# Optimization experiments

Measured on AMD Instinct MI355X. Metric: run time of the kernel, lower is better.

Reference implementation:

```python
import jax, jax.numpy as jnp
import numpy as np

B, T, C, H = 8, 2048, 768, 12
D = C // H

def setup_inputs() -> dict:
    key = jax.random.key(0)
    ks = jax.random.split(key, 5)
    s = 0.02
    return {
        "x": jax.random.normal(ks[0], (B, T, C), dtype=jnp.float32),
        "w_attn": jax.random.normal(ks[1], (C, 3 * C), dtype=jnp.float32) * s,
        "b_attn": jnp.zeros((3 * C,), dtype=jnp.float32),
        "w_proj": jax.random.normal(ks[2], (C, C), dtype=jnp.float32) * s,
        "b_proj": jnp.zeros((C,), dtype=jnp.float32),
    }

def reference(x, w_attn, b_attn, w_proj, b_proj):
    Bx, Tx, Cx = x.shape
    qkv = x @ w_attn + b_attn                       # [B,T,3C]
    q, k, v = jnp.split(qkv, 3, axis=-1)
    # [B,H,T,D]
    q = q.reshape(Bx, Tx, H, D).transpose(0, 2, 1, 3)
    k = k.reshape(Bx, Tx, H, D).transpose(0, 2, 1, 3)
    v = v.reshape(Bx, Tx, H, D).transpose(0, 2, 1, 3)
    scale = 1.0 / jnp.sqrt(jnp.float32(D))
    att = jnp.einsum('bhqd,bhkd->bhqk', q, k) * scale
    causal = jnp.tril(jnp.ones((Tx, Tx), dtype=bool))
    att = jnp.where(causal[None, None], att, -jnp.inf)
    att = jax.nn.softmax(att, axis=-1)
    y = jnp.einsum('bhqk,bhkd->bhqd', att, v)
    y = y.transpose(0, 2, 1, 3).reshape(Bx, Tx, Cx)
    y = y @ w_proj + b_proj
    return y, k, v
```

## Files before the change

### kernel.cpp

```cpp
#include <hip/hip_runtime.h>
#include <hip/hip_bf16.h>
#include <stdint.h>

#define Bz 8
#define Tz 2048
#define Cz 768
#define Hz 12
#define Dz 64
#define Mz (Bz*Tz)
#define N3 (3*Cz)
#define YSZ ((size_t)Mz*Cz)

#define SCL 0.18033688011112042f
#define KVB 64
#define QBLK 128

typedef __bf16 bf16;
typedef __attribute__((ext_vector_type(8))) bf16 bf16x8;
typedef __attribute__((ext_vector_type(4))) bf16 bf16x4;
typedef __attribute__((ext_vector_type(4))) float f32x4;

#define MFMA(A_,B_,C_) __builtin_amdgcn_mfma_f32_16x16x32_bf16(A_,B_,C_,0,0,0)

__device__ __forceinline__ void gll16(const void* g, void* l) {
  __builtin_amdgcn_global_load_lds(
      (const __attribute__((address_space(1))) void*)g,
      (__attribute__((address_space(3))) void*)l, 16, 0, 0);
}

__global__ __launch_bounds__(256) void prep_x(const float* __restrict__ x,
                                              bf16* __restrict__ xb) {
  int i = blockIdx.x*blockDim.x + threadIdx.x;
  int stride = gridDim.x*blockDim.x;
  const float4* x4 = (const float4*)x;
  int n4 = (int)(YSZ/4);
  for (int j = i; j < n4; j += stride) {
    float4 f = x4[j];
    bf16x4 o = { (bf16)f.x, (bf16)f.y, (bf16)f.z, (bf16)f.w };
    *(bf16x4*)(xb + 4*(size_t)j) = o;
  }
}

__global__ __launch_bounds__(256) void transpose_conv(const float* __restrict__ src,
                                                      bf16* __restrict__ dst,
                                                      int R, int Ncol) {
  __shared__ float tile[32][33];
  int bx = blockIdx.x, by = blockIdx.y;
  int tx = threadIdx.x & 31, ty = threadIdx.x >> 5;
  #pragma unroll
  for (int i = 0; i < 4; ++i)
    tile[ty + 8*i][tx] = src[(size_t)(by*32 + ty + 8*i)*Ncol + bx*32 + tx];
  __syncthreads();
  #pragma unroll
  for (int i = 0; i < 4; ++i)
    dst[(size_t)(bx*32 + ty + 8*i)*R + by*32 + tx] = (bf16)tile[tx][ty + 8*i];
}

template<int EPI>
__global__ __launch_bounds__(256) void gemm128(
    const bf16* __restrict__ A, const bf16* __restrict__ Bt,
    int Kdim, int Mtiles, int Ntiles,
    const float* __restrict__ bias,
    bf16* __restrict__ qws, bf16* __restrict__ kws, bf16* __restrict__ vtb,
    float* __restrict__ kout, float* __restrict__ vout,
    float* __restrict__ yout)
{
  __shared__ alignas(16) bf16 sA[2][128*64];
  __shared__ alignas(16) bf16 sB[2][128*64];
  int nwg = Mtiles*Ntiles;
  int bid = blockIdx.x;
  int cpx = nwg >> 3;
  int swz = (bid & 7)*cpx + (bid >> 3);
  int ntile = swz % Ntiles, mtile = swz / Ntiles;
  int tid = threadIdx.x, w = tid >> 6, l = tid & 63;
  int wr = w >> 1, wc = w & 1;
  const int rowBase = mtile*128, colBase = ntile*128;

  f32x4 acc[4][4] = {};

  int rbase = tid >> 3;
  int ch    = tid & 7;
  int swk   = (ch ^ (rbase & 7)) << 3;
  const bf16* gA = A + (size_t)(rowBase + rbase)*Kdim + swk;
  const bf16* gB = Bt + (size_t)(colBase + rbase)*Kdim + swk;

  int lr = l & 15, lg = l >> 4;
  int nK = Kdim >> 6;

  {
    char* lA = (char*)sA[0] + w*1024;
    char* lB = (char*)sB[0] + w*1024;
    #pragma unroll
    for (int p = 0; p < 4; ++p) {
      gll16(gA + (size_t)(p*32)*Kdim, lA + p*4096);
      gll16(gB + (size_t)(p*32)*Kdim, lB + p*4096);
    }
    gA += 64; gB += 64;
  }
  int buf = 0;
  for (int t = 0; t < nK; ++t) {
    if (t + 1 < nK) {
      char* lA = (char*)sA[buf ^ 1] + w*1024;
      char* lB = (char*)sB[buf ^ 1] + w*1024;
      #pragma unroll
      for (int p = 0; p < 4; ++p) {
        gll16(gA + (size_t)(p*32)*Kdim, lA + p*4096);
        gll16(gB + (size_t)(p*32)*Kdim, lB + p*4096);
      }
      gA += 64; gB += 64;
      asm volatile("s_waitcnt vmcnt(8)" ::: "memory");
    } else {
      asm volatile("s_waitcnt vmcnt(0)" ::: "memory");
    }
    __builtin_amdgcn_s_barrier();
    __builtin_amdgcn_sched_barrier(0);
    const char* cA = (const char*)sA[buf];
    const char* cB = (const char*)sB[buf];
    __builtin_amdgcn_s_setprio(1);
    #pragma unroll
    for (int kk = 0; kk < 2; ++kk) {
      bf16x8 af[4], bfr[4];
      int cc = ((kk*4 + lg) ^ (lr & 7)) << 4;
      #pragma unroll
      for (int m = 0; m < 4; ++m)
        af[m] = *(const bf16x8*)(cA + (wr*64 + m*16 + lr)*128 + cc);
      #pragma unroll
      for (int n = 0; n < 4; ++n)
        bfr[n] = *(const bf16x8*)(cB + (wc*64 + n*16 + lr)*128 + cc);
      #pragma unroll
      for (int m = 0; m < 4; ++m)
        #pragma unroll
        for (int n = 0; n < 4; ++n)
          acc[m][n] = MFMA(af[m], bfr[n], acc[m][n]);
    }
    __builtin_amdgcn_s_setprio(0);
    asm volatile("s_waitcnt lgkmcnt(0)" ::: "memory");
    __builtin_amdgcn_s_barrier();
    __builtin_amdgcn_sched_barrier(0);
    buf ^= 1;
  }

  #pragma unroll
  for (int m = 0; m < 4; ++m) {
    #pragma unroll
    for (int n = 0; n < 4; ++n) {
      int gcol = colBase + wc*64 + n*16 + lr;
      float bv = bias[gcol];
      int grow0 = rowBase + wr*64 + m*16 + lg*4;
      if (EPI == 1) {
        #pragma unroll
        for (int r = 0; r < 4; ++r)
          yout[(size_t)(grow0 + r)*Cz + gcol] = acc[m][n][r] + bv;
      } else {
        int which = gcol / Cz;
        int within = gcol - which*Cz;
        int h = within >> 6, d = within & 63;
        int bidx = grow0 >> 11;
        int t0 = grow0 & 2047;
        size_t bhTD = ((size_t)bidx*Hz + h);
        if (which == 0) {
          bf16* qp = qws + (bhTD*Tz + t0)*Dz + d;
          #pragma unroll
          for (int r = 0; r < 4; ++r)
            qp[(size_t)r*Dz] = (bf16)((acc[m][n][r] + bv) * SCL);
        } else if (which == 1) {
          float* kp = kout + (bhTD*Tz + t0)*Dz + d;
          bf16*  kp2 = kws + (bhTD*Tz + t0)*Dz + d;
          #pragma unroll
          for (int r = 0; r < 4; ++r) {
            float v = acc[m][n][r] + bv;
            kp[(size_t)r*Dz] = v;
            kp2[(size_t)r*Dz] = (bf16)v;
          }
        } else {
          float* vp = vout + (bhTD*Tz + t0)*Dz + d;
          bf16x4 pk;
          #pragma unroll
          for (int r = 0; r < 4; ++r) {
            float v = acc[m][n][r] + bv;
            vp[(size_t)r*Dz] = v;
            pk[r] = (bf16)v;
          }
          int ts = (t0 & ~31) | (((t0 >> 2) & 3) << 3) | (((t0 >> 4) & 1) << 2) | (t0 & 3);
          *(bf16x4*)(vtb + (bhTD*Dz + d)*Tz + ts) = pk;
        }
      }
    }
  }
}

__device__ __forceinline__ void stageKV(const bf16* kgb, const bf16* vgb, int kv0,
                                        char* cK, char* cV, int tid, int w) {
  int off = tid*16;
  int row = off >> 7, ch = (off >> 4) & 7;
  int sw = ((ch ^ (row & 7)) << 3);
  gll16(kgb + (size_t)(kv0 + row)*Dz + sw, cK + w*1024);
  gll16(vgb + (size_t)row*Tz + kv0 + sw,   cV + w*1024);
}

__device__ __forceinline__ void attn_tile(
    int kv0, int qminw, int qmaxw, int q_l, int lr, int lg,
    const char* cK, const char* cV,
    const bf16x8& qf0, const bf16x8& qf1,
    f32x4 (&o)[4], float& mrun, float& lrun)
{
  const f32x4 zf = {0.f, 0.f, 0.f, 0.f};
  f32x4 s[4];
  __builtin_amdgcn_s_setprio(1);
  #pragma unroll
  for (int n = 0; n < 4; ++n) {
    int kvb = kv0 + n*16;
    if (kvb <= qmaxw) {
      int row = n*16 + lr;
      int c0 = lg ^ (lr & 7);
      bf16x8 kf0 = *(const bf16x8*)(cK + row*128 + (c0 << 4));
      bf16x8 kf1 = *(const bf16x8*)(cK + row*128 + ((c0 ^ 4) << 4));
      f32x4 t = MFMA(kf0, qf0, zf);
      s[n] = MFMA(kf1, qf1, t);
    } else {
      s[n][0] = -1e30f; s[n][1] = -1e30f; s[n][2] = -1e30f; s[n][3] = -1e30f;
    }
  }
  __builtin_amdgcn_s_setprio(0);
  #pragma unroll
  for (int n = 0; n < 4; ++n) {
    int kvb = kv0 + n*16;
    if (kvb <= qmaxw && kvb + 15 > qminw) {
      #pragma unroll
      for (int r = 0; r < 4; ++r)
        s[n][r] = (kvb + 4*lg + r <= q_l) ? s[n][r] : -1e30f;
    }
  }
  f32x4 a0;
  #pragma unroll
  for (int r = 0; r < 4; ++r)
    a0[r] = fmaxf(fmaxf(s[0][r], s[1][r]), fmaxf(s[2][r], s[3][r]));
  float mx = fmaxf(fmaxf(a0[0], a0[1]), fmaxf(a0[2], a0[3]));
  mx = fmaxf(mx, __shfl_xor(mx, 16));
  mx = fmaxf(mx, __shfl_xor(mx, 32));

  bool skip = __all(mx <= mrun + 8.0f);
  float corr = 1.0f;
  if (!skip) {
    float mnew = fmaxf(mrun, mx);
    corr = exp2f(mrun - mnew);
    mrun = mnew;
  }
  f32x4 acc4 = zf;
  #pragma unroll
  for (int n = 0; n < 4; ++n) {
    #pragma unroll
    for (int r = 0; r < 4; ++r) {
      float e = exp2f(s[n][r] - mrun);
      s[n][r] = e;
      acc4[r] += e;
    }
  }
  float rs = (acc4[0] + acc4[1]) + (acc4[2] + acc4[3]);
  rs += __shfl_xor(rs, 16);
  rs += __shfl_xor(rs, 32);
  if (!skip) {
    lrun = lrun*corr + rs;
    float c0_ = __shfl(corr, 4*lg + 0);
    float c1_ = __shfl(corr, 4*lg + 1);
    float c2_ = __shfl(corr, 4*lg + 2);
    float c3_ = __shfl(corr, 4*lg + 3);
    #pragma unroll
    for (int nd = 0; nd < 4; ++nd) {
      o[nd][0] *= c0_; o[nd][1] *= c1_; o[nd][2] *= c2_; o[nd][3] *= c3_;
    }
  } else {
    lrun += rs;
  }
  __builtin_amdgcn_s_setprio(1);
  #pragma unroll
  for (int kk = 0; kk < 2; ++kk) {
    if (kv0 + kk*32 <= qmaxw) {
      bf16x8 pf;
      pf[0] = (bf16)s[2*kk][0];   pf[1] = (bf16)s[2*kk][1];
      pf[2] = (bf16)s[2*kk][2];   pf[3] = (bf16)s[2*kk][3];
      pf[4] = (bf16)s[2*kk+1][0]; pf[5] = (bf16)s[2*kk+1][1];
      pf[6] = (bf16)s[2*kk+1][2]; pf[7] = (bf16)s[2*kk+1][3];
      int cb = (kk*4 + lg) ^ (lr & 7);
      #pragma unroll
      for (int nd = 0; nd < 4; ++nd) {
        bf16x8 vf = *(const bf16x8*)(cV + (nd*16 + lr)*128 + (cb << 4));
        o[nd] = MFMA(pf, vf, o[nd]);
      }
    }
  }
  __builtin_amdgcn_s_setprio(0);
}

__global__ __launch_bounds__(512, 6) void attn128(
    const bf16* __restrict__ qws, const bf16* __restrict__ kb,
    const bf16* __restrict__ vtb, bf16* __restrict__ yatt)
{
  __shared__ alignas(16) char sK[2][8192];
  __shared__ alignas(16) char sV[2][8192];
  int bid = blockIdx.x;
  int qb = (Tz/QBLK) - 1 - bid/(Bz*Hz);
  int bh = bid % (Bz*Hz);
  int b = bh / Hz, h = bh - b*Hz;
  int tid = threadIdx.x, w = tid >> 6, l = tid & 63;
  int lr = l & 15, lg = l >> 4;
  const int q0 = qb*QBLK;
  const int qminw = q0 + w*16;
  const int qmaxw = qminw + 15;
  const int q_l = qminw + lr;

  const bf16* qbase = qws + ((size_t)bh*Tz + qminw + lr)*Dz + lg*8;
  bf16x8 qf0 = *(const bf16x8*)qbase;
  bf16x8 qf1 = *(const bf16x8*)(qbase + 32);

  f32x4 o[4] = {};
  float mrun = -1e30f, lrun = 0.f;

  const bf16* kgb = kb  + (size_t)bh*Tz*Dz;
  const bf16* vgb = vtb + (size_t)bh*Dz*Tz;

  int nT = 2*qb + 2;
  stageKV(kgb, vgb, 0, sK[0], sV[0], tid, w);
  int buf = 0;
  for (int kt = 0; kt + 1 < nT; ++kt) {
    stageKV(kgb, vgb, (kt + 1)*KVB, sK[buf ^ 1], sV[buf ^ 1], tid, w);
    asm volatile("s_waitcnt vmcnt(2)" ::: "memory");
    __builtin_amdgcn_s_barrier();
    __builtin_amdgcn_sched_barrier(0);
    attn_tile(kt*KVB, qminw, qmaxw, q_l, lr, lg, sK[buf], sV[buf],
              qf0, qf1, o, mrun, lrun);
    asm volatile("s_waitcnt lgkmcnt(0)" ::: "memory");
    __builtin_amdgcn_s_barrier();
    __builtin_amdgcn_sched_barrier(0);
    buf ^= 1;
  }
  asm volatile("s_waitcnt vmcnt(0)" ::: "memory");
  __builtin_amdgcn_s_barrier();
  __builtin_amdgcn_sched_barrier(0);
  attn_tile((nT - 1)*KVB, qminw, qmaxw, q_l, lr, lg, sK[buf], sV[buf],
            qf0, qf1, o, mrun, lrun);

  float inv = 1.0f / lrun;
  float i0 = __shfl(inv, 4*lg + 0);
  float i1 = __shfl(inv, 4*lg + 1);
  float i2 = __shfl(inv, 4*lg + 2);
  float i3 = __shfl(inv, 4*lg + 3);
  #pragma unroll
  for (int nd = 0; nd < 4; ++nd) {
    int d = nd*16 + lr;
    int t0 = q0 + w*16 + lg*4;
    bf16* yp = yatt + ((size_t)(b*Tz + t0))*Cz + h*Dz + d;
    yp[0*Cz]   = (bf16)(o[nd][0] * i0);
    yp[1*Cz]   = (bf16)(o[nd][1] * i1);
    yp[2*Cz]   = (bf16)(o[nd][2] * i2);
    yp[3*Cz]   = (bf16)(o[nd][3] * i3);
  }
}

extern "C" void kernel_launch(void* const* d_in, const int* in_sizes, int n_in,
                              void* d_out, int out_size, void* d_ws, size_t ws_size,
                              hipStream_t stream) {
  const float* x      = (const float*)d_in[0];
  const float* w_attn = (const float*)d_in[1];
  const float* b_attn = (const float*)d_in[2];
  const float* w_proj = (const float*)d_in[3];
  const float* b_proj = (const float*)d_in[4];

  float* y    = (float*)d_out;
  float* kout = y + YSZ;
  float* vout = y + 2*YSZ;

  char* ws = (char*)d_ws;
  bf16* xb   = (bf16*)ws;
  bf16* qws  = (bf16*)(ws + 25165824);
  bf16* kb   = (bf16*)(ws + 50331648);
  bf16* vtb  = (bf16*)(ws + 75497472);
  bf16* wtA  = (bf16*)(ws + 100663296);
  bf16* wtP  = (bf16*)(ws + 104202240);
  bf16* yatt = xb;

  prep_x<<<2048, 256, 0, stream>>>(x, xb);
  transpose_conv<<<dim3(N3/32, Cz/32), 256, 0, stream>>>(w_attn, wtA, Cz, N3);
  transpose_conv<<<dim3(Cz/32, Cz/32), 256, 0, stream>>>(w_proj, wtP, Cz, Cz);

  gemm128<0><<<dim3((Mz/128)*(N3/128)), 256, 0, stream>>>(
      xb, wtA, Cz, Mz/128, N3/128, b_attn, qws, kb, vtb, kout, vout, nullptr);

  attn128<<<dim3((Tz/QBLK)*(Bz*Hz)), 512, 0, stream>>>(qws, kb, vtb, yatt);

  gemm128<1><<<dim3((Mz/128)*(Cz/128)), 256, 0, stream>>>(
      yatt, wtP, Cz, Mz/128, Cz/128, b_proj, nullptr, nullptr, nullptr,
      nullptr, nullptr, y);
}
```

Measured before the change: 261.5 us.

## Compute softmax row sums via MFMA with ones vector and unroll double-buffer loop

Replaces the per-lane exp accumulation and cross-lane shuffle reduction of the softmax denominator with an extra MFMA of the bf16 probabilities against a ones vector, so the row sum lands in the same layout as the output accumulator. The sum is now built from bf16-rounded probabilities, which keeps it consistent with the P·V product but slightly changes numerics. The K/V double-buffer loop is unrolled by two with fixed buffer pointers and incrementing global addresses. This removes the stageKV address recomputation and the buffer-index select, at the cost of larger code.

```diff
diff --git a/kernel.cpp b/kernel.cpp
--- a/kernel.cpp
+++ b/kernel.cpp
@@ -189,20 +189,11 @@
   }
 }
 
-__device__ __forceinline__ void stageKV(const bf16* kgb, const bf16* vgb, int kv0,
-                                        char* cK, char* cV, int tid, int w) {
-  int off = tid*16;
-  int row = off >> 7, ch = (off >> 4) & 7;
-  int sw = ((ch ^ (row & 7)) << 3);
-  gll16(kgb + (size_t)(kv0 + row)*Dz + sw, cK + w*1024);
-  gll16(vgb + (size_t)row*Tz + kv0 + sw,   cV + w*1024);
-}
-
 __device__ __forceinline__ void attn_tile(
     int kv0, int qminw, int qmaxw, int q_l, int lr, int lg,
     const char* cK, const char* cV,
-    const bf16x8& qf0, const bf16x8& qf1,
-    f32x4 (&o)[4], float& mrun, float& lrun)
+    const bf16x8& qf0, const bf16x8& qf1, const bf16x8& ones,
+    f32x4 (&o)[4], f32x4& lsum, float& mrun)
 {
   const f32x4 zf = {0.f, 0.f, 0.f, 0.f};
   f32x4 s[4];
@@ -240,27 +231,10 @@
   mx = fmaxf(mx, __shfl_xor(mx, 32));
 
   bool skip = __all(mx <= mrun + 8.0f);
-  float corr = 1.0f;
   if (!skip) {
     float mnew = fmaxf(mrun, mx);
-    corr = exp2f(mrun - mnew);
+    float corr = exp2f(mrun - mnew);
     mrun = mnew;
-  }
-  f32x4 acc4 = zf;
-  #pragma unroll
-  for (int n = 0; n < 4; ++n) {
-    #pragma unroll
-    for (int r = 0; r < 4; ++r) {
-      float e = exp2f(s[n][r] - mrun);
-      s[n][r] = e;
-      acc4[r] += e;
-    }
-  }
-  float rs = (acc4[0] + acc4[1]) + (acc4[2] + acc4[3]);
-  rs += __shfl_xor(rs, 16);
-  rs += __shfl_xor(rs, 32);
-  if (!skip) {
-    lrun = lrun*corr + rs;
     float c0_ = __shfl(corr, 4*lg + 0);
     float c1_ = __shfl(corr, 4*lg + 1);
     float c2_ = __shfl(corr, 4*lg + 2);
@@ -269,8 +243,13 @@
     for (int nd = 0; nd < 4; ++nd) {
       o[nd][0] *= c0_; o[nd][1] *= c1_; o[nd][2] *= c2_; o[nd][3] *= c3_;
     }
-  } else {
-    lrun += rs;
+    lsum[0] *= c0_; lsum[1] *= c1_; lsum[2] *= c2_; lsum[3] *= c3_;
+  }
+  #pragma unroll
+  for (int n = 0; n < 4; ++n) {
+    #pragma unroll
+    for (int r = 0; r < 4; ++r)
+      s[n][r] = exp2f(s[n][r] - mrun);
   }
   __builtin_amdgcn_s_setprio(1);
   #pragma unroll
@@ -281,6 +260,7 @@
       pf[2] = (bf16)s[2*kk][2];   pf[3] = (bf16)s[2*kk][3];
       pf[4] = (bf16)s[2*kk+1][0]; pf[5] = (bf16)s[2*kk+1][1];
       pf[6] = (bf16)s[2*kk+1][2]; pf[7] = (bf16)s[2*kk+1][3];
+      lsum = MFMA(pf, ones, lsum);
       int cb = (kk*4 + lg) ^ (lr & 7);
       #pragma unroll
       for (int nd = 0; nd < 4; ++nd) {
@@ -313,47 +293,62 @@
   bf16x8 qf0 = *(const bf16x8*)qbase;
   bf16x8 qf1 = *(const bf16x8*)(qbase + 32);
 
+  bf16 onev = (bf16)1.0f;
+  bf16x8 ones = { onev, onev, onev, onev, onev, onev, onev, onev };
+
   f32x4 o[4] = {};
-  float mrun = -1e30f, lrun = 0.f;
-
-  const bf16* kgb = kb  + (size_t)bh*Tz*Dz;
-  const bf16* vgb = vtb + (size_t)bh*Dz*Tz;
+  f32x4 lsum = {0.f, 0.f, 0.f, 0.f};
+  float mrun = -1e30f;
+
+  int srow = tid >> 3;
+  int ssw  = ((tid & 7) ^ (srow & 7)) << 3;
+  const bf16* kp = kb  + (size_t)bh*Tz*Dz + (size_t)srow*Dz + ssw;
+  const bf16* vp = vtb + (size_t)bh*Dz*Tz + (size_t)srow*Tz + ssw;
+  char* dK0 = sK[0] + w*1024;  char* dV0 = sV[0] + w*1024;
+  char* dK1 = sK[1] + w*1024;  char* dV1 = sV[1] + w*1024;
 
   int nT = 2*qb + 2;
-  stageKV(kgb, vgb, 0, sK[0], sV[0], tid, w);
-  int buf = 0;
-  for (int kt = 0; kt + 1 < nT; ++kt) {
-    stageKV(kgb, vgb, (kt + 1)*KVB, sK[buf ^ 1], sV[buf ^ 1], tid, w);
+  gll16(kp, dK0); gll16(vp, dV0); kp += (size_t)KVB*Dz; vp += KVB;
+
+  for (int kt = 0; kt < nT; kt += 2) {
+    gll16(kp, dK1); gll16(vp, dV1); kp += (size_t)KVB*Dz; vp += KVB;
     asm volatile("s_waitcnt vmcnt(2)" ::: "memory");
     __builtin_amdgcn_s_barrier();
     __builtin_amdgcn_sched_barrier(0);
-    attn_tile(kt*KVB, qminw, qmaxw, q_l, lr, lg, sK[buf], sV[buf],
-              qf0, qf1, o, mrun, lrun);
+    attn_tile(kt*KVB, qminw, qmaxw, q_l, lr, lg, sK[0], sV[0],
+              qf0, qf1, ones, o, lsum, mrun);
     asm volatile("s_waitcnt lgkmcnt(0)" ::: "memory");
     __builtin_amdgcn_s_barrier();
     __builtin_amdgcn_sched_barrier(0);
-    buf ^= 1;
-  }
-  asm volatile("s_waitcnt vmcnt(0)" ::: "memory");
-  __builtin_amdgcn_s_barrier();
-  __builtin_amdgcn_sched_barrier(0);
-  attn_tile((nT - 1)*KVB, qminw, qmaxw, q_l, lr, lg, sK[buf], sV[buf],
-            qf0, qf1, o, mrun, lrun);
-
-  float inv = 1.0f / lrun;
-  float i0 = __shfl(inv, 4*lg + 0);
-  float i1 = __shfl(inv, 4*lg + 1);
-  float i2 = __shfl(inv, 4*lg + 2);
-  float i3 = __shfl(inv, 4*lg + 3);
+    if (kt + 2 < nT) {
+      gll16(kp, dK0); gll16(vp, dV0); kp += (size_t)KVB*Dz; vp += KVB;
+      asm volatile("s_waitcnt vmcnt(2)" ::: "memory");
+    } else {
+      asm volatile("s_waitcnt vmcnt(0)" ::: "memory");
+    }
+    __builtin_amdgcn_s_barrier();
+    __builtin_amdgcn_sched_barrier(0);
+    attn_tile((kt + 1)*KVB, qminw, qmaxw, q_l, lr, lg, sK[1], sV[1],
+              qf0, qf1, ones, o, lsum, mrun);
+    if (kt + 2 < nT) {
+      asm volatile("s_waitcnt lgkmcnt(0)" ::: "memory");
+      __builtin_amdgcn_s_barrier();
+      __builtin_amdgcn_sched_barrier(0);
+    }
+  }
+
+  f32x4 inv;
+  #pragma unroll
+  for (int r = 0; r < 4; ++r) inv[r] = 1.0f / lsum[r];
   #pragma unroll
   for (int nd = 0; nd < 4; ++nd) {
     int d = nd*16 + lr;
     int t0 = q0 + w*16 + lg*4;
     bf16* yp = yatt + ((size_t)(b*Tz + t0))*Cz + h*Dz + d;
-    yp[0*Cz]   = (bf16)(o[nd][0] * i0);
-    yp[1*Cz]   = (bf16)(o[nd][1] * i1);
-    yp[2*Cz]   = (bf16)(o[nd][2] * i2);
-    yp[3*Cz]   = (bf16)(o[nd][3] * i3);
+    yp[0*Cz]   = (bf16)(o[nd][0] * inv[0]);
+    yp[1*Cz]   = (bf16)(o[nd][1] * inv[1]);
+    yp[2*Cz]   = (bf16)(o[nd][2] * inv[2]);
+    yp[3*Cz]   = (bf16)(o[nd][3] * inv[3]);
   }
 }
 
```

Result: no change. 266.5 us (+1.9%).
